# Kernel tuning notes

Hardware: AMD Instinct MI355X
Metric: run time of the kernel (lower is better)

## Reference

```python
import jax, jax.numpy as jnp
import numpy as np

EPS = 1e-12


def setup_inputs() -> dict:
    key = jax.random.key(0)
    k1, k2 = jax.random.split(key)
    ide_feats = jax.random.normal(k1, (4096, 256), dtype=jnp.float32)
    u_feats = jax.random.normal(k2, (16384, 256), dtype=jnp.float32)
    return {"ide_feats": ide_feats, "u_feats": u_feats}


def reference(ide_feats, u_feats):
    # euclidean_dist: sqrt(sum((x_i - y_j)^2) + eps) -> [N, M]
    # computed via the GEMM expansion to avoid the [N, M, D] intermediate
    x2 = jnp.sum(ide_feats * ide_feats, axis=-1)[:, None]   # [N, 1]
    y2 = jnp.sum(u_feats * u_feats, axis=-1)[None, :]       # [1, M]
    xy = jnp.einsum('nd,md->nm', ide_feats, u_feats)        # [N, M]
    d2 = jnp.maximum(x2 + y2 - 2.0 * xy, 0.0)
    dists = jnp.sqrt(d2 + EPS)                              # [N, M]
    d = jnp.mean(dists, axis=-1)                            # [N]
    # dist_loss: sum_{i,j} sqrt((d_i - d_j)^2 + eps)
    diff = d[:, None] - d[None, :]                          # [N, N]
    loss = jnp.sum(jnp.sqrt(diff * diff + EPS))
    return loss
```

## Files before the change

### kernel.cpp

```cpp
#include <hip/hip_runtime.h>
#include <hip/hip_bf16.h>
#include <cstdint>

#define N_IDE 4096
#define M_U   16384
#define D_DIM 256
#define EPSF  1e-12f
#define INV_M (1.0f / 16384.0f)

#define CGC   512
#define BK    32
#define SB_ELEMS (CGC * BK)

typedef _Float16 f16x8 __attribute__((ext_vector_type(8)));
typedef float    f32x4 __attribute__((ext_vector_type(4)));

__device__ __forceinline__ void gll16(const void* g, void* l) {
  __builtin_amdgcn_global_load_lds(
      (const __attribute__((address_space(1))) void*)(uintptr_t)g,
      (__attribute__((address_space(3))) void*)(uint32_t)(uintptr_t)l,
      16, 0, 0);
}

__device__ __forceinline__ unsigned short f2h_bits(float f) {
  _Float16 h = (_Float16)f;
  return __builtin_bit_cast(unsigned short, h);
}

__global__ __launch_bounds__(256) void k_conv(const float* __restrict__ ide,
                                              const float* __restrict__ u,
                                              unsigned short* __restrict__ Ah,
                                              unsigned short* __restrict__ Bh,
                                              float* __restrict__ x2,
                                              float* __restrict__ y2) {
  int gw = (blockIdx.x * 256 + threadIdx.x) >> 6;
  int l  = threadIdx.x & 63;
  const float4* src;
  ushort4* dst;
  float* nrm;
  if (gw < N_IDE) {
    src = (const float4*)(ide + (size_t)gw * D_DIM);
    dst = (ushort4*)(Ah + (size_t)gw * D_DIM);
    nrm = x2 + gw;
  } else {
    int r = gw - N_IDE;
    src = (const float4*)(u + (size_t)r * D_DIM);
    dst = (ushort4*)(Bh + (size_t)r * D_DIM);
    nrm = y2 + r;
  }
  float4 v = src[l];
  float s = v.x * v.x + v.y * v.y + v.z * v.z + v.w * v.w;
  ushort4 o;
  o.x = f2h_bits(v.x); o.y = f2h_bits(v.y);
  o.z = f2h_bits(v.z); o.w = f2h_bits(v.w);
  dst[l] = o;
#pragma unroll
  for (int m = 1; m <= 32; m <<= 1) s += __shfl_xor(s, m, 64);
  if (l == 0) *nrm = s;
}

__global__ __launch_bounds__(512, 2) void k_gemm(const unsigned short* __restrict__ Ah,
                                                 const unsigned short* __restrict__ Bh,
                                                 const float* __restrict__ x2,
                                                 const float* __restrict__ y2,
                                                 float* __restrict__ partial) {
  __shared__ __align__(16) unsigned short sA[128 * 256];
  __shared__ __align__(16) unsigned short sB[2 * SB_ELEMS];
  __shared__ float rowacc[4][128];

  const int t    = threadIdx.x;
  const int w    = t >> 6;
  const int l    = t & 63;
  const int wm   = w >> 2, wn = w & 3;
  const int lrow = l & 15;
  const int lhi  = l >> 4;
  const int bx   = blockIdx.x;
  const int by   = blockIdx.y;

  rowacc[t >> 7][t & 127] = 0.f;

#pragma unroll
  for (int i = 0; i < 8; ++i) {
    int L = i * 512 + t;
    int row = L >> 5;
    int p = L & 31;
    int c = (p & 24) | ((p & 7) ^ (row & 7));
    gll16(Ah + (size_t)(by * 128 + row) * D_DIM + c * 8,
          sA + (size_t)(i * 512 + w * 64) * 8);
  }

  auto stageB = [&](int s) {
    const int cgi = (s >> 3) * 8 + bx;
    const int kt  = s & 7;
    const unsigned short* src = Bh + (size_t)cgi * CGC * D_DIM + kt * BK;
    unsigned short* dstb = sB + (size_t)(s & 1) * SB_ELEMS;
#pragma unroll
    for (int j = 0; j < 4; ++j) {
      int L = j * 512 + t;
      int row = L >> 2;
      int c = L & 3;
      gll16(src + (size_t)row * D_DIM + c * 8,
            dstb + (size_t)(j * 512 + w * 64) * 8);
    }
  };

  float4 x2v[4];
#pragma unroll
  for (int mi = 0; mi < 4; ++mi)
    x2v[mi] = *(const float4*)&x2[by * 128 + wm * 64 + mi * 16 + lhi * 4];

  stageB(0);
  __syncthreads();

  for (int cg = 0; cg < 4; ++cg) {
    const int cgi = cg * 8 + bx;

    f32x4 acc[4][8];
#pragma unroll
    for (int mi = 0; mi < 4; ++mi)
#pragma unroll
      for (int ni = 0; ni < 8; ++ni)
        acc[mi][ni] = (f32x4){0.f, 0.f, 0.f, 0.f};

    for (int kt = 0; kt < 8; ++kt) {
      const int s = cg * 8 + kt;
      if (s + 1 < 32) stageB(s + 1);

      f16x8 af[4];
#pragma unroll
      for (int mi = 0; mi < 4; ++mi) {
        int arow = wm * 64 + mi * 16 + lrow;
        int lc   = kt * 4 + lhi;
        int pc   = (lc & 24) | ((lc & 7) ^ (lrow & 7));
        af[mi] = *(const f16x8*)(sA + (size_t)arow * 256 + pc * 8);
      }

      const unsigned short* bbuf = sB + (size_t)(s & 1) * SB_ELEMS;
#pragma unroll
      for (int half = 0; half < 2; ++half) {
        f16x8 bf[4];
#pragma unroll
        for (int nj = 0; nj < 4; ++nj) {
          int brow = wn * 128 + (half * 4 + nj) * 16 + lrow;
          bf[nj] = *(const f16x8*)(bbuf + (size_t)brow * BK + lhi * 8);
        }
#pragma unroll
        for (int mi = 0; mi < 4; ++mi)
#pragma unroll
          for (int nj = 0; nj < 4; ++nj)
            acc[mi][half * 4 + nj] =
                __builtin_amdgcn_mfma_f32_16x16x32_f16(af[mi], bf[nj],
                                                       acc[mi][half * 4 + nj], 0, 0, 0);
      }
      __syncthreads();
    }

    float yv[8];
#pragma unroll
    for (int ni = 0; ni < 8; ++ni)
      yv[ni] = y2[cgi * CGC + wn * 128 + ni * 16 + lrow];

#pragma unroll
    for (int mi = 0; mi < 4; ++mi) {
      float xr[4] = {x2v[mi].x, x2v[mi].y, x2v[mi].z, x2v[mi].w};
#pragma unroll
      for (int rr = 0; rr < 4; ++rr) {
        float ssum = 0.f;
#pragma unroll
        for (int ni = 0; ni < 8; ++ni) {
          float d2 = xr[rr] + yv[ni] - 2.0f * acc[mi][ni][rr];
          d2 = fmaxf(d2, 0.0f);
          ssum += __builtin_amdgcn_sqrtf(d2 + EPSF);
        }
        ssum += __shfl_xor(ssum, 1, 64);
        ssum += __shfl_xor(ssum, 2, 64);
        ssum += __shfl_xor(ssum, 4, 64);
        ssum += __shfl_xor(ssum, 8, 64);
        if (lrow == 0)
          rowacc[wn][wm * 64 + mi * 16 + lhi * 4 + rr] += ssum;
      }
    }
  }

  __syncthreads();
  if (t < 128)
    partial[(size_t)bx * N_IDE + by * 128 + t] =
        rowacc[0][t] + rowacc[1][t] + rowacc[2][t] + rowacc[3][t];
}

__global__ __launch_bounds__(256) void k_loss(const float* __restrict__ partial,
                                              float* __restrict__ out) {
  __shared__ float sd[N_IDE];
  __shared__ float wsum[4];
  int t = threadIdx.x;
  for (int k = t; k < N_IDE; k += 256) {
    float s = 0.f;
#pragma unroll
    for (int b = 0; b < 8; ++b) s += partial[(size_t)b * N_IDE + k];
    sd[k] = s;
  }
  __syncthreads();
  int tid = blockIdx.x * 256 + t;
  int i   = tid >> 4;
  int jl  = tid & 15;
  float di = sd[i];
  float s  = 0.f;
  for (int k = 0; k < 256; ++k) {
    float diff = (di - sd[jl + k * 16]) * INV_M;
    s += __builtin_amdgcn_sqrtf(diff * diff + EPSF);
  }
#pragma unroll
  for (int m = 1; m <= 32; m <<= 1) s += __shfl_xor(s, m, 64);
  if ((t & 63) == 0) wsum[t >> 6] = s;
  __syncthreads();
  if (t == 0) atomicAdd(out, wsum[0] + wsum[1] + wsum[2] + wsum[3]);
}

extern "C" void kernel_launch(void* const* d_in, const int* in_sizes, int n_in,
                              void* d_out, int out_size, void* d_ws, size_t ws_size,
                              hipStream_t stream) {
  (void)in_sizes; (void)n_in; (void)out_size; (void)ws_size;
  const float* ide = (const float*)d_in[0];
  const float* u   = (const float*)d_in[1];
  float* out = (float*)d_out;

  char* ws = (char*)d_ws;
  size_t off = 0;
  unsigned short* Ah = (unsigned short*)(ws + off); off += (size_t)N_IDE * D_DIM * 2;
  unsigned short* Bh = (unsigned short*)(ws + off); off += (size_t)M_U  * D_DIM * 2;
  float* x2      = (float*)(ws + off); off += (size_t)N_IDE * 4;
  float* y2      = (float*)(ws + off); off += (size_t)M_U * 4;
  float* partial = (float*)(ws + off); off += (size_t)8 * N_IDE * 4;

  hipMemsetAsync(d_out, 0, sizeof(float), stream);
  k_conv<<<(N_IDE + M_U) / 4, 256, 0, stream>>>(ide, u, Ah, Bh, x2, y2);
  k_gemm<<<dim3(8, 32), 512, 0, stream>>>(Ah, Bh, x2, y2, partial);
  k_loss<<<256, 256, 0, stream>>>(partial, out);
}
```

Before: 128.0 us.

## Load B fragments straight to registers with double buffering, drop B LDS staging

The GEMM kernel stops staging B tiles through shared memory with global-to-LDS copies and barriers. Each wave now loads its B fragments directly from global memory into a pair of register buffers, alternating between them to hide latency. A is stored in LDS already in fragment order, so the swizzle math goes away, and the per-k-step __syncthreads is removed. The output zeroing moves from a memset into the conversion kernel. In exchange there is more register pressure and redundant global B loads across the two wm waves, which may cost occupancy and L2 bandwidth.

```diff
diff --git a/kernel.cpp b/kernel.cpp
--- a/kernel.cpp
+++ b/kernel.cpp
@@ -8,10 +8,6 @@
 #define EPSF  1e-12f
 #define INV_M (1.0f / 16384.0f)
 
-#define CGC   512
-#define BK    32
-#define SB_ELEMS (CGC * BK)
-
 typedef _Float16 f16x8 __attribute__((ext_vector_type(8)));
 typedef float    f32x4 __attribute__((ext_vector_type(4)));
 
@@ -32,7 +28,9 @@
                                               unsigned short* __restrict__ Ah,
                                               unsigned short* __restrict__ Bh,
                                               float* __restrict__ x2,
-                                              float* __restrict__ y2) {
+                                              float* __restrict__ y2,
+                                              float* __restrict__ out0) {
+  if (blockIdx.x == 0 && threadIdx.x == 0) *out0 = 0.f;
   int gw = (blockIdx.x * 256 + threadIdx.x) >> 6;
   int l  = threadIdx.x & 63;
   const float4* src;
@@ -65,7 +63,6 @@
                                                  const float* __restrict__ y2,
                                                  float* __restrict__ partial) {
   __shared__ __align__(16) unsigned short sA[128 * 256];
-  __shared__ __align__(16) unsigned short sB[2 * SB_ELEMS];
   __shared__ float rowacc[4][128];
 
   const int t    = threadIdx.x;
@@ -80,28 +77,18 @@
   rowacc[t >> 7][t & 127] = 0.f;
 
 #pragma unroll
-  for (int i = 0; i < 8; ++i) {
-    int L = i * 512 + t;
-    int row = L >> 5;
-    int p = L & 31;
-    int c = (p & 24) | ((p & 7) ^ (row & 7));
-    gll16(Ah + (size_t)(by * 128 + row) * D_DIM + c * 8,
+  for (int i = 0; i < 8; ++i)
+    gll16(Ah + (size_t)(by * 128 + w * 16 + lrow) * D_DIM + (i * 4 + lhi) * 8,
           sA + (size_t)(i * 512 + w * 64) * 8);
-  }
-
-  auto stageB = [&](int s) {
+
+  const unsigned short* Bbase = Bh + (size_t)(wn * 128 + lrow) * D_DIM + lhi * 8;
+  auto loadB = [&](f16x8* buf, int s) {
     const int cgi = (s >> 3) * 8 + bx;
     const int kt  = s & 7;
-    const unsigned short* src = Bh + (size_t)cgi * CGC * D_DIM + kt * BK;
-    unsigned short* dstb = sB + (size_t)(s & 1) * SB_ELEMS;
-#pragma unroll
-    for (int j = 0; j < 4; ++j) {
-      int L = j * 512 + t;
-      int row = L >> 2;
-      int c = L & 3;
-      gll16(src + (size_t)row * D_DIM + c * 8,
-            dstb + (size_t)(j * 512 + w * 64) * 8);
-    }
+    const unsigned short* p = Bbase + (size_t)cgi * 512 * D_DIM + kt * 32;
+#pragma unroll
+    for (int ni = 0; ni < 8; ++ni)
+      buf[ni] = *(const f16x8*)(p + (size_t)ni * 16 * D_DIM);
   };
 
   float4 x2v[4];
@@ -109,7 +96,9 @@
   for (int mi = 0; mi < 4; ++mi)
     x2v[mi] = *(const float4*)&x2[by * 128 + wm * 64 + mi * 16 + lhi * 4];
 
-  stageB(0);
+  f16x8 bf0[8], bf1[8];
+  loadB(bf0, 0);
+
   __syncthreads();
 
   for (int cg = 0; cg < 4; ++cg) {
@@ -122,43 +111,32 @@
       for (int ni = 0; ni < 8; ++ni)
         acc[mi][ni] = (f32x4){0.f, 0.f, 0.f, 0.f};
 
-    for (int kt = 0; kt < 8; ++kt) {
-      const int s = cg * 8 + kt;
-      if (s + 1 < 32) stageB(s + 1);
-
+    auto step = [&](int kt, const f16x8* bf) {
       f16x8 af[4];
 #pragma unroll
-      for (int mi = 0; mi < 4; ++mi) {
-        int arow = wm * 64 + mi * 16 + lrow;
-        int lc   = kt * 4 + lhi;
-        int pc   = (lc & 24) | ((lc & 7) ^ (lrow & 7));
-        af[mi] = *(const f16x8*)(sA + (size_t)arow * 256 + pc * 8);
-      }
-
-      const unsigned short* bbuf = sB + (size_t)(s & 1) * SB_ELEMS;
-#pragma unroll
-      for (int half = 0; half < 2; ++half) {
-        f16x8 bf[4];
-#pragma unroll
-        for (int nj = 0; nj < 4; ++nj) {
-          int brow = wn * 128 + (half * 4 + nj) * 16 + lrow;
-          bf[nj] = *(const f16x8*)(bbuf + (size_t)brow * BK + lhi * 8);
-        }
-#pragma unroll
-        for (int mi = 0; mi < 4; ++mi)
-#pragma unroll
-          for (int nj = 0; nj < 4; ++nj)
-            acc[mi][half * 4 + nj] =
-                __builtin_amdgcn_mfma_f32_16x16x32_f16(af[mi], bf[nj],
-                                                       acc[mi][half * 4 + nj], 0, 0, 0);
-      }
-      __syncthreads();
+      for (int mi = 0; mi < 4; ++mi)
+        af[mi] = *(const f16x8*)(sA + (size_t)(((kt * 8) + wm * 4 + mi) * 64 + l) * 8);
+#pragma unroll
+      for (int mi = 0; mi < 4; ++mi)
+#pragma unroll
+        for (int ni = 0; ni < 8; ++ni)
+          acc[mi][ni] = __builtin_amdgcn_mfma_f32_16x16x32_f16(af[mi], bf[ni],
+                                                               acc[mi][ni], 0, 0, 0);
+    };
+
+#pragma unroll
+    for (int ktp = 0; ktp < 4; ++ktp) {
+      const int s = cg * 8 + ktp * 2;
+      loadB(bf1, s + 1);
+      step(ktp * 2, bf0);
+      loadB(bf0, (s + 2 < 32) ? s + 2 : 31);
+      step(ktp * 2 + 1, bf1);
     }
 
     float yv[8];
 #pragma unroll
     for (int ni = 0; ni < 8; ++ni)
-      yv[ni] = y2[cgi * CGC + wn * 128 + ni * 16 + lrow];
+      yv[ni] = y2[cgi * 512 + wn * 128 + ni * 16 + lrow];
 
 #pragma unroll
     for (int mi = 0; mi < 4; ++mi) {
@@ -232,8 +210,7 @@
   float* y2      = (float*)(ws + off); off += (size_t)M_U * 4;
   float* partial = (float*)(ws + off); off += (size_t)8 * N_IDE * 4;
 
-  hipMemsetAsync(d_out, 0, sizeof(float), stream);
-  k_conv<<<(N_IDE + M_U) / 4, 256, 0, stream>>>(ide, u, Ah, Bh, x2, y2);
+  k_conv<<<(N_IDE + M_U) / 4, 256, 0, stream>>>(ide, u, Ah, Bh, x2, y2, out);
   k_gemm<<<dim3(8, 32), 512, 0, stream>>>(Ah, Bh, x2, y2, partial);
   k_loss<<<256, 256, 0, stream>>>(partial, out);
 }
```

Result: slower. 192.2 us (+50.2%).
